# Optimization experiments

Measured on AMD Instinct MI355X. Metric: run time of the kernel, lower is better.

The kernel has to match this reference:

```python
import jax, jax.numpy as jnp
import numpy as np

SCALES = (0.25, 0.125, 0.0625, 0.03125)
OUT = 7   # output_size
SR = 2    # sampling_ratio


def _to_rois(boxes):
    # boxes: [B, N, 4] -> rois: [B*N, 5] = (batch_id, x1, y1, x2, y2)
    B, N, _ = boxes.shape
    ids = jnp.broadcast_to(jnp.arange(B, dtype=boxes.dtype)[:, None, None], (B, N, 1))
    return jnp.concatenate([ids, boxes], axis=-1).reshape(B * N, 5)


def _roi_align(feat, rois, scale, out_size, sr):
    #   roi coords scaled by spatial_scale, roi w/h clamped to >= 1,
    #   sr x sr bilinear samples per output bin, averaged.
    B, C, H, W = feat.shape
    R = rois.shape[0]
    dt = feat.dtype
    bidx = rois[:, 0].astype(jnp.int32)
    x1 = rois[:, 1] * scale
    y1 = rois[:, 2] * scale
    x2 = rois[:, 3] * scale
    y2 = rois[:, 4] * scale
    rw = jnp.maximum(x2 - x1, 1.0)
    rh = jnp.maximum(y2 - y1, 1.0)
    # sample coordinate (k+0.5)/sr in units of bin size, k in [0, out_size*sr)
    g = (jnp.arange(out_size * sr, dtype=dt) + 0.5) / sr          # [PS]
    ys = y1[:, None] + (rh / out_size)[:, None] * g               # [R, PS]
    xs = x1[:, None] + (rw / out_size)[:, None] * g               # [R, PS]
    Hf = jnp.asarray(H, dt); Wf = jnp.asarray(W, dt)
    vy = (ys >= -1.0) & (ys <= Hf)                                # out-of-range -> 0
    vx = (xs >= -1.0) & (xs <= Wf)
    yc = jnp.clip(ys, 0.0, Hf - 1.0)
    xc = jnp.clip(xs, 0.0, Wf - 1.0)
    y0 = jnp.floor(yc).astype(jnp.int32)
    x0 = jnp.floor(xc).astype(jnp.int32)
    y1i = jnp.minimum(y0 + 1, H - 1)
    x1i = jnp.minimum(x0 + 1, W - 1)
    ly = yc - y0.astype(dt); lx = xc - x0.astype(dt)
    hy = 1.0 - ly; hx = 1.0 - lx
    b = bidx[:, None, None]                                       # [R,1,1]
    Y0 = y0[:, :, None]; Y1 = y1i[:, :, None]                     # [R,PS,1]
    X0 = x0[:, None, :]; X1 = x1i[:, None, :]                     # [R,1,PS]
    # advanced indexing with a middle slice -> [R, PS, PS, C]
    v00 = feat[b, :, Y0, X0]
    v01 = feat[b, :, Y0, X1]
    v10 = feat[b, :, Y1, X0]
    v11 = feat[b, :, Y1, X1]
    wy0 = hy[:, :, None, None]; wy1 = ly[:, :, None, None]
    wx0 = hx[:, None, :, None]; wx1 = lx[:, None, :, None]
    val = v00 * (wy0 * wx0) + v01 * (wy0 * wx1) + v10 * (wy1 * wx0) + v11 * (wy1 * wx1)
    valid = (vy[:, :, None] & vx[:, None, :])[..., None]
    val = jnp.where(valid, val, jnp.zeros((), dt))
    # average sr x sr samples per bin: [R, P, S, P, S, C] -> [R, P, P, C]
    val = val.reshape(R, out_size, sr, out_size, sr, C).mean(axis=(2, 4))
    return jnp.transpose(val, (0, 3, 1, 2))                       # [R, C, P, P]


def setup_inputs() -> dict:
    key = jax.random.key(0)
    ks = jax.random.split(key, 5)
    B, C, N = 2, 256, 512
    img_h, img_w = 800.0, 1216.0
    x0 = jax.random.normal(ks[0], (B, C, 200, 304), jnp.float32)
    x1 = jax.random.normal(ks[1], (B, C, 100, 152), jnp.float32)
    x2 = jax.random.normal(ks[2], (B, C, 50, 76), jnp.float32)
    x3 = jax.random.normal(ks[3], (B, C, 25, 38), jnp.float32)
    u = jax.random.uniform(ks[4], (B, N, 4), jnp.float32)
    bx1 = u[..., 0] * (img_w - 17.0)
    by1 = u[..., 1] * (img_h - 17.0)
    bw = 16.0 + u[..., 2] * 240.0
    bh = 16.0 + u[..., 3] * 240.0
    bx2 = jnp.minimum(bx1 + bw, img_w - 1.0)
    by2 = jnp.minimum(by1 + bh, img_h - 1.0)
    boxes = jnp.stack([bx1, by1, bx2, by2], axis=-1)
    return {"x0": x0, "x1": x1, "x2": x2, "x3": x3, "boxes": boxes}


def reference(x0, x1, x2, x3, boxes):
    rois = _to_rois(boxes)
    feats = (x0, x1, x2, x3)
    return tuple(_roi_align(f, rois, s, OUT, SR) for f, s in zip(feats, SCALES))
```

## Files before the change

### kernel.cpp

```cpp
#include <hip/hip_runtime.h>


#define OUTSZ 7
#define NBIN  49
#define NSAMP 196
#define ROI_STRIDE 12544u
#define LVL_STRIDE 12845056u

typedef float f2v __attribute__((ext_vector_type(2)));

__device__ __forceinline__ f2v load_f2(const float* p) {
    f2v v;
    __builtin_memcpy(&v, p, 8);
    return v;
}

__global__ __launch_bounds__(256)
void roi_align_all_levels(const float* __restrict__ f0,
                          const float* __restrict__ f1,
                          const float* __restrict__ f2,
                          const float* __restrict__ f3,
                          const float* __restrict__ boxes,
                          float* __restrict__ out)
{
    __shared__ int   sD0[NSAMP];
    __shared__ int   sD1[NSAMP];
    __shared__ float sW0[NSAMP];
    __shared__ float sW1[NSAMP];
    __shared__ float sW2[NSAMP];
    __shared__ float sW3[NSAMP];

    const int r   = blockIdx.x;
    const int lvl = blockIdx.y;
    const int t   = threadIdx.x;

    int H, W; float scale; const float* feat;
    switch (lvl) {
      case 0:  H = 200; W = 304; scale = 0.25f;    feat = f0; break;
      case 1:  H = 100; W = 152; scale = 0.125f;   feat = f1; break;
      case 2:  H = 50;  W = 76;  scale = 0.0625f;  feat = f2; break;
      default: H = 25;  W = 38;  scale = 0.03125f; feat = f3; break;
    }
    const unsigned HW = (unsigned)(H * W);
    const int b = r >> 9;

    if (t < NSAMP) {
        const float bx1 = boxes[r * 4 + 0] * scale;
        const float by1 = boxes[r * 4 + 1] * scale;
        const float bx2 = boxes[r * 4 + 2] * scale;
        const float by2 = boxes[r * 4 + 3] * scale;
        const float rw  = fmaxf(bx2 - bx1, 1.0f);
        const float rh  = fmaxf(by2 - by1, 1.0f);

        const int bin = t >> 2, sub = t & 3;
        const int ph = bin / 7, pw = bin % 7;
        const int ky = 2 * ph + (sub >> 1);
        const int kx = 2 * pw + (sub & 1);

        const float gy = ((float)ky + 0.5f) * 0.5f;
        const float gx = ((float)kx + 0.5f) * 0.5f;
        const float ys = by1 + (rh / 7.0f) * gy;
        const float xs = bx1 + (rw / 7.0f) * gx;

        const float Hf = (float)H, Wf = (float)W;
        const bool vy = (ys >= -1.0f) && (ys <= Hf);
        const bool vx = (xs >= -1.0f) && (xs <= Wf);

        const float yc = fminf(fmaxf(ys, 0.0f), Hf - 1.0f);
        const float xc = fminf(fmaxf(xs, 0.0f), Wf - 1.0f);
        const int y0 = (int)yc;
        const int x0 = (int)xc;
        const int y1i = min(y0 + 1, H - 1);
        const float ly = yc - (float)y0, lx = xc - (float)x0;
        const float hy = 1.0f - ly, hx = 1.0f - lx;

        int px; float wxA, wxB;
        if (x0 < W - 1) { px = x0;     wxA = hx;   wxB = lx;   }
        else            { px = W - 2;  wxA = 0.0f; wxB = 1.0f; }

        const float vm = (vy && vx) ? 0.25f : 0.0f;

        const int s = sub * NBIN + bin;
        sD0[s] = y0  * W + px;
        sD1[s] = y1i * W + px;
        sW0[s] = hy * wxA * vm;
        sW1[s] = hy * wxB * vm;
        sW2[s] = ly * wxA * vm;
        sW3[s] = ly * wxB * vm;
    }
    __syncthreads();

    const float* base = feat + (size_t)b * (size_t)(256u * HW);
    float* o = out + (size_t)lvl * LVL_STRIDE + (size_t)r * ROI_STRIDE;

    #pragma unroll 1
    for (int i = 0; i < 48; i += 2) {
        const int itemA = i * 256 + t;
        const int itemB = itemA + 256;
        const unsigned cA = (unsigned)itemA / 49u;
        const unsigned cB = (unsigned)itemB / 49u;
        const int binA = itemA - (int)cA * 49;
        const int binB = itemB - (int)cB * 49;
        const float* pA = base + (size_t)cA * HW;
        const float* pB = base + (size_t)cB * HW;

        float accA = 0.0f, accB = 0.0f;
        #pragma unroll
        for (int sub = 0; sub < 4; ++sub) {
            const int sA = sub * NBIN + binA;
            const int sB = sub * NBIN + binB;
            const f2v a0 = load_f2(pA + sD0[sA]);
            const f2v a1 = load_f2(pA + sD1[sA]);
            const f2v b0 = load_f2(pB + sD0[sB]);
            const f2v b1 = load_f2(pB + sD1[sB]);
            accA += a0.x * sW0[sA] + a0.y * sW1[sA]
                  + a1.x * sW2[sA] + a1.y * sW3[sA];
            accB += b0.x * sW0[sB] + b0.y * sW1[sB]
                  + b1.x * sW2[sB] + b1.y * sW3[sB];
        }
        o[itemA] = accA;
        o[itemB] = accB;
    }
    {
        const int item = 48 * 256 + t;
        const unsigned c = (unsigned)item / 49u;
        const int bin = item - (int)c * 49;
        const float* p = base + (size_t)c * HW;
        float acc = 0.0f;
        #pragma unroll
        for (int sub = 0; sub < 4; ++sub) {
            const int s = sub * NBIN + bin;
            const f2v a0 = load_f2(p + sD0[s]);
            const f2v a1 = load_f2(p + sD1[s]);
            acc += a0.x * sW0[s] + a0.y * sW1[s]
                 + a1.x * sW2[s] + a1.y * sW3[s];
        }
        o[item] = acc;
    }
}

extern "C" void kernel_launch(void* const* d_in, const int* in_sizes, int n_in,
                              void* d_out, int out_size, void* d_ws, size_t ws_size,
                              hipStream_t stream) {
    const float* f0    = (const float*)d_in[0];
    const float* f1    = (const float*)d_in[1];
    const float* f2    = (const float*)d_in[2];
    const float* f3    = (const float*)d_in[3];
    const float* boxes = (const float*)d_in[4];
    float* out = (float*)d_out;

    dim3 grid(1024, 4);
    roi_align_all_levels<<<grid, 256, 0, stream>>>(f0, f1, f2, f3, boxes, out);
}
```

Before: 622.5 us.

## Transpose features to NHWC in workspace and gather channel-contiguous bilinear samples

Adds a tiled NCHW-to-NHWC transpose of each pyramid level into the workspace. A new ROI gather kernel then reads 256 contiguous channels per sample point with float4 loads. Results are staged in shared memory and written out in the NCHW output order. This replaces scattered per-channel gathers with coalesced loads, at the cost of an extra full read and write of every feature map per call. The old kernel remains as a fallback when the workspace is too small.

```diff
diff --git a/kernel.cpp b/kernel.cpp
--- a/kernel.cpp
+++ b/kernel.cpp
@@ -8,11 +8,145 @@
 #define LVL_STRIDE 12845056u
 
 typedef float f2v __attribute__((ext_vector_type(2)));
+typedef float f4v __attribute__((ext_vector_type(4)));
+
+#define WS_BYTES 165376000ull
+
+__global__ __launch_bounds__(256)
+void nchw_to_nhwc(const float* __restrict__ src, float* __restrict__ dst, int HW)
+{
+    __shared__ float tile[64 * 257];
+    const int t  = threadIdx.x;
+    const int p0 = blockIdx.x * 64;
+    const int b  = blockIdx.y;
+    const float* s = src + (size_t)b * 256u * (size_t)HW;
+    float* d       = dst + (size_t)b * (size_t)HW * 256u;
+
+    const int pl4 = (t & 15) * 4;
+    const int ch  = t >> 4;
+    const int p   = p0 + pl4;
+
+    #pragma unroll 1
+    for (int cc = 0; cc < 16; ++cc) {
+        const int c = cc * 16 + ch;
+        if (p + 3 < HW) {
+            const f4v v = *reinterpret_cast<const f4v*>(s + (size_t)c * HW + p);
+            tile[(pl4 + 0) * 257 + c] = v.x;
+            tile[(pl4 + 1) * 257 + c] = v.y;
+            tile[(pl4 + 2) * 257 + c] = v.z;
+            tile[(pl4 + 3) * 257 + c] = v.w;
+        } else {
+            for (int j = 0; j < 4; ++j)
+                if (p + j < HW) tile[(pl4 + j) * 257 + c] = s[(size_t)c * HW + p + j];
+        }
+    }
+    __syncthreads();
+
+    #pragma unroll 1
+    for (int i = 0; i < 64; ++i) {
+        const int pp = p0 + i;
+        if (pp < HW) d[(size_t)pp * 256u + t] = tile[i * 257 + t];
+    }
+}
+
+__global__ __launch_bounds__(256)
+void roi_gather_nhwc(const float* __restrict__ ws, const float* __restrict__ boxes,
+                     float* __restrict__ out)
+{
+    __shared__ float obuf[NBIN * 257];
+
+    const int r   = blockIdx.x;
+    const int lvl = blockIdx.y;
+    const int t   = threadIdx.x;
+    const int wv  = t >> 6;
+    const int l   = t & 63;
+
+    int H, W; float scale; size_t off;
+    switch (lvl) {
+      case 0:  H = 200; W = 304; scale = 0.25f;    off = 0u;        break;
+      case 1:  H = 100; W = 152; scale = 0.125f;   off = 31129600u; break;
+      case 2:  H = 50;  W = 76;  scale = 0.0625f;  off = 38912000u; break;
+      default: H = 25;  W = 38;  scale = 0.03125f; off = 40857600u; break;
+    }
+    const int HW = H * W;
+    const int b  = r >> 9;
+    const float* base = ws + off + (size_t)b * (size_t)HW * 256u;
+
+    const float bx1 = boxes[r * 4 + 0] * scale;
+    const float by1 = boxes[r * 4 + 1] * scale;
+    const float bx2 = boxes[r * 4 + 2] * scale;
+    const float by2 = boxes[r * 4 + 3] * scale;
+    const float rw  = fmaxf(bx2 - bx1, 1.0f);
+    const float rh  = fmaxf(by2 - by1, 1.0f);
+    const float bw7 = rw * (1.0f / 7.0f);
+    const float bh7 = rh * (1.0f / 7.0f);
+    const float Hf = (float)H, Wf = (float)W;
+
+    #pragma unroll 1
+    for (int bin = wv; bin < NBIN; bin += 4) {
+        const int ph = bin / 7;
+        const int pw = bin - ph * 7;
+        f4v acc = {0.0f, 0.0f, 0.0f, 0.0f};
+
+        #pragma unroll
+        for (int sub = 0; sub < 4; ++sub) {
+            const int ky = 2 * ph + (sub >> 1);
+            const int kx = 2 * pw + (sub & 1);
+            const float ys = by1 + bh7 * (((float)ky + 0.5f) * 0.5f);
+            const float xs = bx1 + bw7 * (((float)kx + 0.5f) * 0.5f);
+
+            const bool vy = (ys >= -1.0f) && (ys <= Hf);
+            const bool vx = (xs >= -1.0f) && (xs <= Wf);
+
+            const float yc = fminf(fmaxf(ys, 0.0f), Hf - 1.0f);
+            const float xc = fminf(fmaxf(xs, 0.0f), Wf - 1.0f);
+            const int y0 = (int)yc;
+            const int x0 = (int)xc;
+            const int y1i = min(y0 + 1, H - 1);
+            const float ly = yc - (float)y0, lx = xc - (float)x0;
+            const float hy = 1.0f - ly, hx = 1.0f - lx;
+
+            int px; float wxA, wxB;
+            if (x0 < W - 1) { px = x0;     wxA = hx;   wxB = lx;   }
+            else            { px = W - 2;  wxA = 0.0f; wxB = 1.0f; }
+
+            const float vm  = (vy && vx) ? 0.25f : 0.0f;
+            const float w00 = hy * wxA * vm;
+            const float w01 = hy * wxB * vm;
+            const float w10 = ly * wxA * vm;
+            const float w11 = ly * wxB * vm;
+
+            const float* r0 = base + (size_t)(y0  * W + px) * 256u;
+            const float* r1 = base + (size_t)(y1i * W + px) * 256u;
+
+            const f4v a0 = *reinterpret_cast<const f4v*>(r0 + 4 * l);
+            const f4v b0 = *reinterpret_cast<const f4v*>(r0 + 256 + 4 * l);
+            const f4v a1 = *reinterpret_cast<const f4v*>(r1 + 4 * l);
+            const f4v b1 = *reinterpret_cast<const f4v*>(r1 + 256 + 4 * l);
+
+            acc += a0 * w00 + b0 * w01 + a1 * w10 + b1 * w11;
+        }
+
+        const int s = bin * 257 + 4 * l;
+        obuf[s + 0] = acc.x;
+        obuf[s + 1] = acc.y;
+        obuf[s + 2] = acc.z;
+        obuf[s + 3] = acc.w;
+    }
+    __syncthreads();
+
+    float* o = out + (size_t)lvl * LVL_STRIDE + (size_t)r * ROI_STRIDE;
+    #pragma unroll 1
+    for (int k = 0; k < NBIN; ++k) {
+        const int item = k * 256 + t;
+        const unsigned c = (unsigned)item / 49u;
+        const int bin = item - (int)c * 49;
+        o[item] = obuf[bin * 257 + (int)c];
+    }
+}
 
 __device__ __forceinline__ f2v load_f2(const float* p) {
-    f2v v;
-    __builtin_memcpy(&v, p, 8);
-    return v;
+    f2v v; __builtin_memcpy(&v, p, 8); return v;
 }
 
 __global__ __launch_bounds__(256)
@@ -149,6 +283,15 @@
     const float* boxes = (const float*)d_in[4];
     float* out = (float*)d_out;
 
-    dim3 grid(1024, 4);
-    roi_align_all_levels<<<grid, 256, 0, stream>>>(f0, f1, f2, f3, boxes, out);
-}
+    if (d_ws != nullptr && ws_size >= WS_BYTES) {
+        float* w = (float*)d_ws;
+        nchw_to_nhwc<<<dim3(950, 2), 256, 0, stream>>>(f0, w + 0u,        60800);
+        nchw_to_nhwc<<<dim3(238, 2), 256, 0, stream>>>(f1, w + 31129600u, 15200);
+        nchw_to_nhwc<<<dim3(60,  2), 256, 0, stream>>>(f2, w + 38912000u, 3800);
+        nchw_to_nhwc<<<dim3(15,  2), 256, 0, stream>>>(f3, w + 40857600u, 950);
+        roi_gather_nhwc<<<dim3(1024, 4), 256, 0, stream>>>(w, boxes, out);
+    } else {
+        dim3 grid(1024, 4);
+        roi_align_all_levels<<<grid, 256, 0, stream>>>(f0, f1, f2, f3, boxes, out);
+    }
+}
```

New measurement: 533.6 us. 14.3% less time.
